# Kernel optimization log

Measured on AMD Instinct MI355X. Metric: run time of the kernel, lower is better.

The kernel has to match this reference:

```python
import jax, jax.numpy as jnp
import numpy as np

V, B, S = 24, 8, 512
H1, H2 = 128, 64          # mechanism hidden sizes
SH1, SH2 = 256, 128       # structure learner hidden sizes
IH = 32                   # independence test hidden
P = V * V                 # all ordered pairs (diag unused)


def _lin(k, fi, fo):
    return jax.random.normal(k, (fi, fo), dtype=jnp.float32) / np.sqrt(fi)


def setup_inputs() -> dict:
    key = jax.random.key(0)
    ks = jax.random.split(key, 18)
    data = jax.random.normal(ks[0], (B, S, V), dtype=jnp.float32)
    # structure learner: V*V -> 256 -> 128 -> V*V
    sW1, sb1 = _lin(ks[1], V * V, SH1), jnp.zeros((SH1,), jnp.float32)
    sW2, sb2 = _lin(ks[2], SH1, SH2), jnp.zeros((SH2,), jnp.float32)
    sW3, sb3 = _lin(ks[3], SH2, V * V), jnp.zeros((V * V,), jnp.float32)
    # per-variable causal mechanisms: (V-1) -> 128 -> 64 -> 1, batched over V
    mW1 = jax.random.normal(ks[4], (V, V - 1, H1), jnp.float32) / np.sqrt(V - 1)
    mb1 = jnp.zeros((V, H1), jnp.float32)
    mW2 = jax.random.normal(ks[5], (V, H1, H2), jnp.float32) / np.sqrt(H1)
    mb2 = jnp.zeros((V, H2), jnp.float32)
    mW3 = jax.random.normal(ks[6], (V, H2, 1), jnp.float32) / np.sqrt(H2)
    mb3 = jnp.zeros((V, 1), jnp.float32)
    # per-pair independence tests: 2 -> 32 -> 1, batched over P pairs
    iW1 = jax.random.normal(ks[7], (P, 2, IH), jnp.float32) / np.sqrt(2)
    ib1 = jnp.zeros((P, IH), jnp.float32)
    iW2 = jax.random.normal(ks[8], (P, IH, 1), jnp.float32) / np.sqrt(IH)
    ib2 = jnp.zeros((P, 1), jnp.float32)
    return dict(data=data, sW1=sW1, sb1=sb1, sW2=sW2, sb2=sb2, sW3=sW3, sb3=sb3,
                mW1=mW1, mb1=mb1, mW2=mW2, mb2=mb2, mW3=mW3, mb3=mb3,
                iW1=iW1, ib1=ib1, iW2=iW2, ib2=ib2)


# constant gather index: others[v] = all variable indices except v (order preserved)
_OTHERS = np.array([[j for j in range(V) if j != v] for v in range(V)])  # [V, V-1]
_II = np.repeat(np.arange(V), V)  # pair -> i
_JJ = np.tile(np.arange(V), V)    # pair -> j


def reference(data, sW1, sb1, sW2, sb2, sW3, sb3,
              mW1, mb1, mW2, mb2, mW3, mb3,
              iW1, ib1, iW2, ib2):
    relu, sig = jax.nn.relu, jax.nn.sigmoid
    b, s, v = data.shape

    # ---- correlations (vectorized torch.corrcoef over all pairs) ----
    avg = data.mean(axis=0)                       # [S, V]
    c = avg - avg.mean(axis=0, keepdims=True)
    cov = c.T @ c                                 # [V, V]
    std = jnp.sqrt(jnp.diag(cov))
    corr = jnp.abs(cov / (std[:, None] * std[None, :]))
    corr = jnp.where(jnp.isnan(corr), 0.0, corr)
    corr = corr * (1.0 - jnp.eye(v, dtype=corr.dtype))

    # ---- structure learner (dropout in eval mode = identity) ----
    h = relu(corr.reshape(1, -1) @ sW1 + sb1)
    h = relu(h @ sW2 + sb2)
    adj = sig(h @ sW3 + sb3).reshape(v, v)
    adj = jnp.triu(adj, k=1)                      # DAG: strict upper triangle

    # ---- causal mechanisms: parent-masked other-vars -> small MLP per var ----
    parent_mask = adj > 0.5                       # parent_mask[p, child]
    x_others = data[:, :, _OTHERS]                # [B, S, V, V-1]
    pmask = parent_mask[_OTHERS, np.arange(V)[:, None]]  # [V, V-1]
    xin = x_others * pmask.astype(data.dtype)[None, None]
    hm = relu(jnp.einsum('bsvf,vfh->bsvh', xin, mW1) + mb1)
    hm = relu(jnp.einsum('bsvh,vhg->bsvg', hm, mW2) + mb2)
    pred = (jnp.einsum('bsvg,vgo->bsvo', hm, mW3) + mb3)[..., 0]  # [B, S, V]
    has_parent = parent_mask.any(axis=0)          # [V]
    predictions = jnp.where(has_parent[None, None, :], pred, data)

    # ---- independence tests: per-pair 2->32->1 MLP, mean over all samples ----
    flatd = data.reshape(b * s, v)                # [N, V]
    tin = jnp.stack([flatd[:, _II], flatd[:, _JJ]], axis=-1)  # [N, P, 2]
    tin = tin.transpose(1, 0, 2)                  # [P, N, 2]
    hi = relu(jnp.einsum('pnf,pfh->pnh', tin, iW1) + ib1[:, None, :])
    si = sig(jnp.einsum('pnh,pho->pno', hi, iW2) + ib2[:, None, :])
    ind_scores = si.mean(axis=(1, 2)).reshape(v, v)

    return adj, predictions, ind_scores
```

## Files before the change

kernel.cpp:

```cpp
#include <hip/hip_runtime.h>
#include <math.h>

#define NV 24
#define NB 8
#define NS 512
#define NTOK 4096
#define H1 128
#define H2 64
#define SH1 256
#define SH2 128
#define IH 32
#define NP 576

typedef short bf16x8 __attribute__((ext_vector_type(8)));
typedef float f32x4 __attribute__((ext_vector_type(4)));

__device__ __forceinline__ short f2bf(float f) {
    union { float f; unsigned u; } x; x.f = f;
    unsigned r = x.u + 0x7fffu + ((x.u >> 16) & 1u);
    return (short)(r >> 16);
}

__device__ __forceinline__ float blk_reduce(float x, float* red, int t) {
#pragma unroll
    for (int o = 32; o > 0; o >>= 1) x += __shfl_xor(x, o);
    if ((t & 63) == 0) red[t >> 6] = x;
    __syncthreads();
    float r = red[0] + red[1] + red[2] + red[3];
    __syncthreads();
    return r;
}


__global__ __launch_bounds__(256) void k_prep(
    const float* __restrict__ data, float* __restrict__ dataT,
    const float* __restrict__ sW1, const float* __restrict__ sW2,
    const float* __restrict__ sW3,
    float* __restrict__ sW1T, float* __restrict__ sW2T, float* __restrict__ sW3T,
    const float* __restrict__ mW1, const float* __restrict__ mW2,
    const float* __restrict__ iW1, const float* __restrict__ ib1,
    const float* __restrict__ iW2,
    float* __restrict__ scratch) {
    __shared__ __align__(16) char L[16900];
    const int u = blockIdx.x, t = threadIdx.x;
    if (u < 384) {
        int idx = u * 256 + t;
        int n = idx / NV, v = idx % NV;
        dataT[v * NTOK + n] = data[idx];
        return;
    }
    if (u < 446) {
        float (*T)[65] = (float (*)[65])L;
        int rb = u - 384;
        const float* src; float* dst; int R, C, ti, tj;
        if (rb < 36)      { src = sW1; dst = sW1T; R = 576; C = 256; ti = rb >> 2;        tj = rb & 3; }
        else if (rb < 44) { src = sW2; dst = sW2T; R = 256; C = 128; ti = (rb - 36) >> 1; tj = (rb - 36) & 1; }
        else              { src = sW3; dst = sW3T; R = 128; C = 576; ti = (rb - 44) / 9;  tj = (rb - 44) % 9; }
        const int col = t & 63, rq = t >> 6;
#pragma unroll
        for (int i = 0; i < 16; ++i) {
            int row = i * 4 + rq;
            T[row][col] = src[(ti * 64 + row) * C + tj * 64 + col];
        }
        __syncthreads();
#pragma unroll
        for (int i = 0; i < 16; ++i) {
            int row = i * 4 + rq;
            dst[(tj * 64 + row) * R + ti * 64 + col] = T[col][row];
        }
        return;
    }
    const int wb = u - 446;
    float acc = 0.f;
    const float4* srcs[5] = { (const float4*)mW1, (const float4*)mW2,
                              (const float4*)iW1, (const float4*)ib1,
                              (const float4*)iW2 };
    const int len4[5] = { NV * 23 * H1 / 4, NV * H1 * H2 / 4,
                          NP * 2 * IH / 4, NP * IH / 4, NP * IH / 4 };
#pragma unroll
    for (int a = 0; a < 5; ++a) {
        const float4* p = srcs[a];
        const int n4 = len4[a];
        for (int idx = wb * 256 + t; idx < n4; idx += 128 * 256) {
            float4 v = p[idx];
            acc += v.x + v.y + v.z + v.w;
        }
    }
    float* red = (float*)L;
    acc = blk_reduce(acc, red, t);
    if (t == 0) scratch[wb] = acc;
}

__global__ __launch_bounds__(256) void k_cov(const float* __restrict__ dataT,
                                             float* __restrict__ cov) {
    __shared__ float red[256];
    const int bx = blockIdx.x;
    const int t = threadIdx.x;
    int i = bx / NV, j = bx % NV;
    const float* ri = dataT + i * NTOK;
    const float* rj = dataT + j * NTOK;
    float ai0 = 0.f, ai1 = 0.f, aj0 = 0.f, aj1 = 0.f;
#pragma unroll
    for (int b = 0; b < NB; ++b) {
        ai0 += ri[b * NS + t];       ai1 += ri[b * NS + t + 256];
        aj0 += rj[b * NS + t];       aj1 += rj[b * NS + t + 256];
    }
    ai0 *= 0.125f; ai1 *= 0.125f; aj0 *= 0.125f; aj1 *= 0.125f;
    float si = blk_reduce(ai0 + ai1, red, t);
    float sj = blk_reduce(aj0 + aj1, red, t);
    float mi = si * (1.f / NS), mj = sj * (1.f / NS);
    float sd = (ai0 - mi) * (aj0 - mj) + (ai1 - mi) * (aj1 - mj);
    sd = blk_reduce(sd, red, t);
    if (t == 0) cov[bx] = sd;
}

__global__ __launch_bounds__(256) void k_adj1(
    const float* __restrict__ cov, const float* __restrict__ sW1T,
    const float* __restrict__ sb1, float* __restrict__ h1out) {
    __shared__ float corrL[NP];
    __shared__ float stdL[NV];
    __shared__ float red[256];
    const int o = blockIdx.x, t = threadIdx.x;
    if (t < NV) stdL[t] = sqrtf(cov[t * (NV + 1)]);
    __syncthreads();
    for (int k = t; k < NP; k += 256) {
        int i = k / NV, j = k % NV;
        float q = fabsf(cov[k] / (stdL[i] * stdL[j]));
        if (isnan(q)) q = 0.f;
        if (i == j) q = 0.f;
        corrL[k] = q;
    }
    __syncthreads();
    const float* w = sW1T + o * 576;
    float w0 = w[t], w1 = w[256 + t];
    float w2 = (t < 64) ? w[512 + t] : 0.f;
    float c2 = (t < 64) ? corrL[512 + t] : 0.f;
    float a = corrL[t] * w0 + corrL[256 + t] * w1 + c2 * w2;
    a = blk_reduce(a, red, t);
    if (t == 0) h1out[o] = fmaxf(a + sb1[o], 0.f);
}

__global__ __launch_bounds__(256) void k_adj2(
    const float* __restrict__ h1, const float* __restrict__ sW2T,
    const float* __restrict__ sb2, float* __restrict__ h2out) {
    __shared__ float red[256];
    const int o = blockIdx.x, t = threadIdx.x;
    float a = h1[t] * sW2T[o * 256 + t];
    a = blk_reduce(a, red, t);
    if (t == 0) h2out[o] = fmaxf(a + sb2[o], 0.f);
}

__global__ __launch_bounds__(256) void k_adj3(
    const float* __restrict__ h2, const float* __restrict__ sW3T,
    const float* __restrict__ sb3, float* __restrict__ out_adj) {
    __shared__ float red[256];
    const int oo = blockIdx.x, t = threadIdx.x;
    float a = (t < SH2) ? h2[t] * sW3T[oo * 128 + t] : 0.f;
    a = blk_reduce(a, red, t);
    if (t == 0) {
        float sg = 1.f / (1.f + expf(-(a + sb3[oo])));
        int i = oo / NV, j = oo % NV;
        out_adj[oo] = (j > i) ? sg : 0.f;
    }
}

__global__ __launch_bounds__(256) void k_predind(
    const float* __restrict__ data,
    const float* __restrict__ mW1, const float* __restrict__ mb1,
    const float* __restrict__ mW2, const float* __restrict__ mb2,
    const float* __restrict__ mW3, const float* __restrict__ mb3,
    const float* __restrict__ adj, float* __restrict__ out_pred,
    const float* __restrict__ dataT,
    const float* __restrict__ iW1, const float* __restrict__ ib1,
    const float* __restrict__ iW2, const float* __restrict__ ib2,
    float* __restrict__ out_ind) {
    __shared__ __align__(16) char L[34816];
    const int bx = blockIdx.x;
    const int t = threadIdx.x;

    if (bx < 768) {
        const int v = bx % NV;
        const int chunk = bx / NV;

        bool hp = false;
#pragma unroll
        for (int r = 0; r < NV; ++r) hp = hp || (adj[r * NV + v] > 0.5f);
        if (!hp) {
            if (t < 128) {
                int tok = chunk * 128 + t;
                out_pred[tok * NV + v] = data[tok * NV + v];
            }
            return;
        }
        short* Xl = (short*)L;
        short* WH = (short*)(L + 10240);
        short* W1B = WH;
        short* W2B = WH + 4096;
        short* Hl = WH;

        if (t < 128) {
            int tok = chunk * 128 + t;
            const float4* dr4 = (const float4*)(data + tok * NV);
            float d[24];
#pragma unroll
            for (int q = 0; q < 6; ++q) {
                float4 uu = dr4[q];
                d[q * 4 + 0] = uu.x; d[q * 4 + 1] = uu.y; d[q * 4 + 2] = uu.z; d[q * 4 + 3] = uu.w;
            }
            short xr[32];
#pragma unroll
            for (int j = 0; j < 23; ++j) {
                int src = j + (j >= v ? 1 : 0);
                xr[j] = f2bf(d[src]);
            }
            xr[23] = f2bf(1.0f);
#pragma unroll
            for (int j = 24; j < 32; ++j) xr[j] = 0;
            short* xp = Xl + t * 40;
#pragma unroll
            for (int q = 0; q < 4; ++q)
                *(bf16x8*)(xp + q * 8) = *(bf16x8*)(xr + q * 8);
        }
        if (t < 184) {
            int k = t >> 3, h8 = (t & 7) * 16;
            int src = k + (k >= v ? 1 : 0);
            float pm = (adj[src * NV + v] > 0.5f) ? 1.f : 0.f;
            const float4* wr = (const float4*)(mW1 + (v * 23 + k) * 128 + h8);
            float wv[16];
#pragma unroll
            for (int q = 0; q < 4; ++q) {
                float4 uu = wr[q];
                wv[q * 4 + 0] = uu.x; wv[q * 4 + 1] = uu.y;
                wv[q * 4 + 2] = uu.z; wv[q * 4 + 3] = uu.w;
            }
            int kb = (k >> 3) & 3, e = k & 7;
#pragma unroll
            for (int q = 0; q < 16; ++q) {
                int h = h8 + q;
                int nt = h >> 4, nn = h & 15;
                W1B[((nt * 4 + kb) * 16 + nn) * 8 + e] = f2bf(wv[q] * pm);
            }
        } else if (t < 200) {
            int h8 = (t - 184) * 8;
            const float4* br = (const float4*)(mb1 + v * 128 + h8);
            float bv[8];
#pragma unroll
            for (int q = 0; q < 2; ++q) {
                float4 uu = br[q];
                bv[q * 4 + 0] = uu.x; bv[q * 4 + 1] = uu.y;
                bv[q * 4 + 2] = uu.z; bv[q * 4 + 3] = uu.w;
            }
#pragma unroll
            for (int q = 0; q < 8; ++q) {
                int h = h8 + q;
                int nt = h >> 4, nn = h & 15;
                W1B[((nt * 4 + 2) * 16 + nn) * 8 + 7] = f2bf(bv[q]);
            }
        }
        if (t < 128) {
            int nt = t >> 4, nn = t & 15;
#pragma unroll
            for (int e = 0; e < 8; ++e)
                W1B[((nt * 4 + 3) * 16 + nn) * 8 + e] = 0;
        }
        {
            int k = t >> 1, n0 = (t & 1) * 32;
            const float4* wr = (const float4*)(mW2 + (v * 128 + k) * 64 + n0);
            float wv[32];
#pragma unroll
            for (int q = 0; q < 8; ++q) {
                float4 uu = wr[q];
                wv[q * 4 + 0] = uu.x; wv[q * 4 + 1] = uu.y;
                wv[q * 4 + 2] = uu.z; wv[q * 4 + 3] = uu.w;
            }
            int s = k >> 5, kb = (k >> 3) & 3, e = k & 7;
#pragma unroll
            for (int q = 0; q < 32; ++q) {
                int n = n0 + q;
                int nt = n >> 4, nn = n & 15;
                W2B[(((s * 4 + nt) * 4 + kb) * 16 + nn) * 8 + e] = f2bf(wv[q]);
            }
        }
        __syncthreads();

        const int lane = t & 63;
        const int wid = t >> 6;
        const int ml = lane & 15;
        const int kb = lane >> 4;
        short* Hw = Hl + wid * 2048;

        bf16x8 w1f[8], w2f[16];
#pragma unroll
        for (int nt = 0; nt < 8; ++nt)
            w1f[nt] = *(bf16x8*)(W1B + (nt * 64 + lane) * 8);
#pragma unroll
        for (int q = 0; q < 16; ++q)
            w2f[q] = *(bf16x8*)(W2B + (q * 64 + lane) * 8);

        float b2r[4], w3r[4];
#pragma unroll
        for (int nt = 0; nt < 4; ++nt) {
            b2r[nt] = mb2[v * 64 + nt * 16 + ml];
            w3r[nt] = mW3[v * 64 + nt * 16 + ml];
        }
        float b3v = mb3[v];

        __syncthreads();

#pragma unroll
        for (int mt = 0; mt < 2; ++mt) {
            int lt = wid * 32 + mt * 16 + ml;
            bf16x8 a1 = *(bf16x8*)(Xl + lt * 40 + kb * 8);
            f32x4 c1[8] = {};
#pragma unroll
            for (int nt = 0; nt < 8; ++nt)
                c1[nt] = __builtin_amdgcn_mfma_f32_16x16x32_bf16(a1, w1f[nt], c1[nt], 0, 0, 0);
#pragma unroll
            for (int nt = 0; nt < 8; ++nt) {
#pragma unroll
                for (int r = 0; r < 4; ++r) {
                    int m = kb * 4 + r;
                    int h = nt * 16 + ml;
                    int bo = (m * 256 + h * 2) ^ ((m & 7) << 4);
                    *(short*)((char*)Hw + bo) = f2bf(fmaxf(c1[nt][r], 0.f));
                }
            }
            f32x4 c2[4] = {};
#pragma unroll
            for (int s = 0; s < 4; ++s) {
                int c0 = s * 32 + kb * 8;
                int bo = (ml * 256 + c0 * 2) ^ ((ml & 7) << 4);
                bf16x8 a2 = *(bf16x8*)((char*)Hw + bo);
#pragma unroll
                for (int nt = 0; nt < 4; ++nt)
                    c2[nt] = __builtin_amdgcn_mfma_f32_16x16x32_bf16(a2, w2f[s * 4 + nt], c2[nt], 0, 0, 0);
            }
            float sacc[4] = {0.f, 0.f, 0.f, 0.f};
#pragma unroll
            for (int nt = 0; nt < 4; ++nt) {
#pragma unroll
                for (int r = 0; r < 4; ++r)
                    sacc[r] += fmaxf(c2[nt][r] + b2r[nt], 0.f) * w3r[nt];
            }
#pragma unroll
            for (int o = 1; o < 16; o <<= 1) {
#pragma unroll
                for (int r = 0; r < 4; ++r)
                    sacc[r] += __shfl_xor(sacc[r], o);
            }
            if (ml == 0) {
                int tokb = chunk * 128 + wid * 32 + mt * 16 + kb * 4;
#pragma unroll
                for (int r = 0; r < 4; ++r)
                    out_pred[(tokb + r) * NV + v] = sacc[r] + b3v;
            }
        }
    } else {
        int p = bx - 768;
        int i = p / NV, j = p % NV;
        float* red = (float*)L;
        float* wl = (float*)L + 256;
        if (t < IH) {
            wl[t]      = iW1[p * 2 * IH + t];
            wl[32 + t] = iW1[p * 2 * IH + IH + t];
            wl[64 + t] = ib1[p * IH + t];
            wl[96 + t] = iW2[p * IH + t];
        }
        __syncthreads();
        float b2v = ib2[p];
        const float* di_p = dataT + i * NTOK;
        const float* dj_p = dataT + j * NTOK;
        float di[16], dj[16], s[16];
#pragma unroll
        for (int q = 0; q < 16; ++q) {
            di[q] = di_p[q * 256 + t];
            dj[q] = dj_p[q * 256 + t];
            s[q] = b2v;
        }
#pragma unroll 4
        for (int h = 0; h < IH; ++h) {
            float w0 = wl[h], w1 = wl[32 + h], bb = wl[64 + h], w2 = wl[96 + h];
#pragma unroll
            for (int q = 0; q < 16; ++q) {
                float a = fmaf(di[q], w0, fmaf(dj[q], w1, bb));
                a = fmaxf(a, 0.f);
                s[q] = fmaf(a, w2, s[q]);
            }
        }
        float acc = 0.f;
#pragma unroll
        for (int q = 0; q < 16; ++q) acc += 1.f / (1.f + expf(-s[q]));
        __syncthreads();
        red[t] = acc;
        __syncthreads();
        for (int st = 128; st > 0; st >>= 1) {
            if (t < st) red[t] += red[t + st];
            __syncthreads();
        }
        if (t == 0) out_ind[p] = red[0] * (1.f / NTOK);
    }
}

extern "C" void kernel_launch(void* const* d_in, const int* in_sizes, int n_in,
                              void* d_out, int out_size, void* d_ws, size_t ws_size,
                              hipStream_t stream) {
    const float* data = (const float*)d_in[0];
    const float* sW1 = (const float*)d_in[1];
    const float* sb1 = (const float*)d_in[2];
    const float* sW2 = (const float*)d_in[3];
    const float* sb2 = (const float*)d_in[4];
    const float* sW3 = (const float*)d_in[5];
    const float* sb3 = (const float*)d_in[6];
    const float* mW1 = (const float*)d_in[7];
    const float* mb1 = (const float*)d_in[8];
    const float* mW2 = (const float*)d_in[9];
    const float* mb2 = (const float*)d_in[10];
    const float* mW3 = (const float*)d_in[11];
    const float* mb3 = (const float*)d_in[12];
    const float* iW1 = (const float*)d_in[13];
    const float* ib1 = (const float*)d_in[14];
    const float* iW2 = (const float*)d_in[15];
    const float* ib2 = (const float*)d_in[16];

    float* out = (float*)d_out;
    float* ws = (float*)d_ws;
    float* ws_cov = ws;
    float* ws_h1 = ws + 576;
    float* ws_h2 = ws + 832;
    float* ws_scratch = ws + 960;
    float* ws_dataT = ws + 2048;
    float* ws_sW1T = ws + 100352;
    float* ws_sW2T = ws + 247808;
    float* ws_sW3T = ws + 280576;

    k_prep<<<dim3(574), dim3(256), 0, stream>>>(data, ws_dataT, sW1, sW2, sW3,
                                                ws_sW1T, ws_sW2T, ws_sW3T,
                                                mW1, mW2, iW1, ib1, iW2,
                                                ws_scratch);
    k_cov<<<dim3(NP), dim3(256), 0, stream>>>(ws_dataT, ws_cov);
    k_adj1<<<dim3(SH1), dim3(256), 0, stream>>>(ws_cov, ws_sW1T, sb1, ws_h1);
    k_adj2<<<dim3(SH2), dim3(256), 0, stream>>>(ws_h1, ws_sW2T, sb2, ws_h2);
    k_adj3<<<dim3(NP), dim3(256), 0, stream>>>(ws_h2, ws_sW3T, sb3, out);
    k_predind<<<dim3(768 + NP), dim3(256), 0, stream>>>(
        data, mW1, mb1, mW2, mb2, mW3, mb3, out, out + NP,
        ws_dataT, iW1, ib1, iW2, ib2, out + NP + NTOK * NV);
}
```

Measured before the change: 43.99 us.

## Fold covariance into prep via partial Gram sums and fuse adj3 into predind

```diff
diff --git a/kernel.cpp b/kernel.cpp
--- a/kernel.cpp
+++ b/kernel.cpp
@@ -40,7 +40,8 @@
     const float* __restrict__ mW1, const float* __restrict__ mW2,
     const float* __restrict__ iW1, const float* __restrict__ ib1,
     const float* __restrict__ iW2,
-    float* __restrict__ scratch) {
+    float* __restrict__ scratch,
+    float* __restrict__ partialS, float* __restrict__ partialG) {
     __shared__ __align__(16) char L[16900];
     const int u = blockIdx.x, t = threadIdx.x;
     if (u < 384) {
@@ -70,62 +71,82 @@
         }
         return;
     }
-    const int wb = u - 446;
-    float acc = 0.f;
-    const float4* srcs[5] = { (const float4*)mW1, (const float4*)mW2,
-                              (const float4*)iW1, (const float4*)ib1,
-                              (const float4*)iW2 };
-    const int len4[5] = { NV * 23 * H1 / 4, NV * H1 * H2 / 4,
-                          NP * 2 * IH / 4, NP * IH / 4, NP * IH / 4 };
-#pragma unroll
-    for (int a = 0; a < 5; ++a) {
-        const float4* p = srcs[a];
-        const int n4 = len4[a];
-        for (int idx = wb * 256 + t; idx < n4; idx += 128 * 256) {
-            float4 v = p[idx];
-            acc += v.x + v.y + v.z + v.w;
-        }
-    }
-    float* red = (float*)L;
-    acc = blk_reduce(acc, red, t);
-    if (t == 0) scratch[wb] = acc;
-}
-
-__global__ __launch_bounds__(256) void k_cov(const float* __restrict__ dataT,
-                                             float* __restrict__ cov) {
-    __shared__ float red[256];
-    const int bx = blockIdx.x;
-    const int t = threadIdx.x;
-    int i = bx / NV, j = bx % NV;
-    const float* ri = dataT + i * NTOK;
-    const float* rj = dataT + j * NTOK;
-    float ai0 = 0.f, ai1 = 0.f, aj0 = 0.f, aj1 = 0.f;
-#pragma unroll
-    for (int b = 0; b < NB; ++b) {
-        ai0 += ri[b * NS + t];       ai1 += ri[b * NS + t + 256];
-        aj0 += rj[b * NS + t];       aj1 += rj[b * NS + t + 256];
-    }
-    ai0 *= 0.125f; ai1 *= 0.125f; aj0 *= 0.125f; aj1 *= 0.125f;
-    float si = blk_reduce(ai0 + ai1, red, t);
-    float sj = blk_reduce(aj0 + aj1, red, t);
-    float mi = si * (1.f / NS), mj = sj * (1.f / NS);
-    float sd = (ai0 - mi) * (aj0 - mj) + (ai1 - mi) * (aj1 - mj);
-    sd = blk_reduce(sd, red, t);
-    if (t == 0) cov[bx] = sd;
+    if (u < 574) {
+        const int wb = u - 446;
+        float acc = 0.f;
+        const float4* srcs[5] = { (const float4*)mW1, (const float4*)mW2,
+                                  (const float4*)iW1, (const float4*)ib1,
+                                  (const float4*)iW2 };
+        const int len4[5] = { NV * 23 * H1 / 4, NV * H1 * H2 / 4,
+                              NP * 2 * IH / 4, NP * IH / 4, NP * IH / 4 };
+#pragma unroll
+        for (int a = 0; a < 5; ++a) {
+            const float4* p = srcs[a];
+            const int n4 = len4[a];
+            for (int idx = wb * 256 + t; idx < n4; idx += 128 * 256) {
+                float4 v = p[idx];
+                acc += v.x + v.y + v.z + v.w;
+            }
+        }
+        float* red = (float*)L;
+        acc = blk_reduce(acc, red, t);
+        if (t == 0) scratch[wb] = acc;
+        return;
+    }
+    const int gb = u - 574;
+    float* avgL = (float*)L;
+    const int s0 = gb * 64;
+    for (int idx = t; idx < 64 * NV; idx += 256) {
+        float a = 0.f;
+#pragma unroll
+        for (int b = 0; b < NB; ++b)
+            a += data[(b * NS + s0) * NV + idx];
+        avgL[idx] = a * 0.125f;
+    }
+    __syncthreads();
+    if (t < NV) {
+        float s = 0.f;
+        for (int ss = 0; ss < 64; ++ss) s += avgL[ss * NV + t];
+        partialS[gb * NV + t] = s;
+    }
+    for (int p = t; p < NP; p += 256) {
+        int i = p / NV, j = p % NV;
+        float g = 0.f;
+        for (int ss = 0; ss < 64; ++ss)
+            g = fmaf(avgL[ss * NV + i], avgL[ss * NV + j], g);
+        partialG[gb * NP + p] = g;
+    }
 }
 
 __global__ __launch_bounds__(256) void k_adj1(
-    const float* __restrict__ cov, const float* __restrict__ sW1T,
-    const float* __restrict__ sb1, float* __restrict__ h1out) {
+    const float* __restrict__ partialG, const float* __restrict__ partialS,
+    const float* __restrict__ sW1T, const float* __restrict__ sb1,
+    float* __restrict__ h1out) {
     __shared__ float corrL[NP];
     __shared__ float stdL[NV];
+    __shared__ float Sv[NV];
     __shared__ float red[256];
     const int o = blockIdx.x, t = threadIdx.x;
-    if (t < NV) stdL[t] = sqrtf(cov[t * (NV + 1)]);
+    if (t < NV) {
+        float s = 0.f;
+#pragma unroll
+        for (int b = 0; b < NB; ++b) s += partialS[b * NV + t];
+        Sv[t] = s;
+    }
+    __syncthreads();
+    for (int k = t; k < NP; k += 256) {
+        float g = 0.f;
+#pragma unroll
+        for (int b = 0; b < NB; ++b) g += partialG[b * NP + k];
+        int i = k / NV, j = k % NV;
+        corrL[k] = g - Sv[i] * Sv[j] * (1.f / NS);
+    }
+    __syncthreads();
+    if (t < NV) stdL[t] = sqrtf(corrL[t * (NV + 1)]);
     __syncthreads();
     for (int k = t; k < NP; k += 256) {
         int i = k / NV, j = k % NV;
-        float q = fabsf(cov[k] / (stdL[i] * stdL[j]));
+        float q = fabsf(corrL[k] / (stdL[i] * stdL[j]));
         if (isnan(q)) q = 0.f;
         if (i == j) q = 0.f;
         corrL[k] = q;
@@ -150,26 +171,14 @@
     if (t == 0) h2out[o] = fmaxf(a + sb2[o], 0.f);
 }
 
-__global__ __launch_bounds__(256) void k_adj3(
-    const float* __restrict__ h2, const float* __restrict__ sW3T,
-    const float* __restrict__ sb3, float* __restrict__ out_adj) {
-    __shared__ float red[256];
-    const int oo = blockIdx.x, t = threadIdx.x;
-    float a = (t < SH2) ? h2[t] * sW3T[oo * 128 + t] : 0.f;
-    a = blk_reduce(a, red, t);
-    if (t == 0) {
-        float sg = 1.f / (1.f + expf(-(a + sb3[oo])));
-        int i = oo / NV, j = oo % NV;
-        out_adj[oo] = (j > i) ? sg : 0.f;
-    }
-}
-
 __global__ __launch_bounds__(256) void k_predind(
     const float* __restrict__ data,
     const float* __restrict__ mW1, const float* __restrict__ mb1,
     const float* __restrict__ mW2, const float* __restrict__ mb2,
     const float* __restrict__ mW3, const float* __restrict__ mb3,
-    const float* __restrict__ adj, float* __restrict__ out_pred,
+    const float* __restrict__ h2, const float* __restrict__ sW3T,
+    const float* __restrict__ sb3,
+    float* __restrict__ out_adj, float* __restrict__ out_pred,
     const float* __restrict__ dataT,
     const float* __restrict__ iW1, const float* __restrict__ ib1,
     const float* __restrict__ iW2, const float* __restrict__ ib2,
@@ -182,9 +191,43 @@
         const int v = bx % NV;
         const int chunk = bx / NV;
 
+        float* P3 = (float*)L;
+        float* maskL = (float*)L + 192;
+        {
+            const int r3 = t >> 3, kq3 = t & 7;
+            if (r3 < NV) {
+                float a = 0.f;
+                if (r3 < v) {
+                    const float* w = sW3T + (r3 * NV + v) * 128 + kq3 * 16;
+                    const float* hp2 = h2 + kq3 * 16;
+#pragma unroll
+                    for (int kk = 0; kk < 16; ++kk)
+                        a = fmaf(hp2[kk], w[kk], a);
+                }
+                P3[r3 * 8 + kq3] = a;
+            }
+        }
+        __syncthreads();
+        if (t < NV) {
+            float s = 0.f;
+#pragma unroll
+            for (int q = 0; q < 8; ++q) s += P3[t * 8 + q];
+            float sg = 1.f / (1.f + expf(-(s + sb3[t * NV + v])));
+            maskL[t] = (t < v && sg > 0.5f) ? 1.f : 0.f;
+        }
+        __syncthreads();
         bool hp = false;
 #pragma unroll
-        for (int r = 0; r < NV; ++r) hp = hp || (adj[r * NV + v] > 0.5f);
+        for (int r = 0; r < NV; ++r) hp = hp || (maskL[r] > 0.5f);
+        float pm_reg = 0.f;
+        int src1 = 0;
+        if (t < 184) {
+            int k = t >> 3;
+            src1 = k + (k >= v ? 1 : 0);
+            pm_reg = maskL[src1];
+        }
+        __syncthreads();
+
         if (!hp) {
             if (t < 128) {
                 int tok = chunk * 128 + t;
@@ -223,8 +266,6 @@
         }
         if (t < 184) {
             int k = t >> 3, h8 = (t & 7) * 16;
-            int src = k + (k >= v ? 1 : 0);
-            float pm = (adj[src * NV + v] > 0.5f) ? 1.f : 0.f;
             const float4* wr = (const float4*)(mW1 + (v * 23 + k) * 128 + h8);
             float wv[16];
 #pragma unroll
@@ -238,7 +279,7 @@
             for (int q = 0; q < 16; ++q) {
                 int h = h8 + q;
                 int nt = h >> 4, nn = h & 15;
-                W1B[((nt * 4 + kb) * 16 + nn) * 8 + e] = f2bf(wv[q] * pm);
+                W1B[((nt * 4 + kb) * 16 + nn) * 8 + e] = f2bf(wv[q] * pm_reg);
             }
         } else if (t < 200) {
             int h8 = (t - 184) * 8;
@@ -355,7 +396,7 @@
                     out_pred[(tokb + r) * NV + v] = sacc[r] + b3v;
             }
         }
-    } else {
+    } else if (bx < 1344) {
         int p = bx - 768;
         int i = p / NV, j = p % NV;
         float* red = (float*)L;
@@ -398,6 +439,16 @@
             __syncthreads();
         }
         if (t == 0) out_ind[p] = red[0] * (1.f / NTOK);
+    } else {
+        float* red = (float*)L;
+        const int oo = bx - 1344;
+        float a = (t < SH2) ? h2[t] * sW3T[oo * 128 + t] : 0.f;
+        a = blk_reduce(a, red, t);
+        if (t == 0) {
+            float sg = 1.f / (1.f + expf(-(a + sb3[oo])));
+            int i = oo / NV, j = oo % NV;
+            out_adj[oo] = (j > i) ? sg : 0.f;
+        }
     }
 }
 
@@ -424,24 +475,23 @@
 
     float* out = (float*)d_out;
     float* ws = (float*)d_ws;
-    float* ws_cov = ws;
     float* ws_h1 = ws + 576;
     float* ws_h2 = ws + 832;
     float* ws_scratch = ws + 960;
-    float* ws_dataT = ws + 2048;
-    float* ws_sW1T = ws + 100352;
-    float* ws_sW2T = ws + 247808;
-    float* ws_sW3T = ws + 280576;
-
-    k_prep<<<dim3(574), dim3(256), 0, stream>>>(data, ws_dataT, sW1, sW2, sW3,
+    float* ws_pS = ws + 1088;
+    float* ws_pG = ws + 1280;
+    float* ws_dataT = ws + 8192;
+    float* ws_sW1T = ws + 106496;
+    float* ws_sW2T = ws + 253952;
+    float* ws_sW3T = ws + 286720;
+
+    k_prep<<<dim3(582), dim3(256), 0, stream>>>(data, ws_dataT, sW1, sW2, sW3,
                                                 ws_sW1T, ws_sW2T, ws_sW3T,
                                                 mW1, mW2, iW1, ib1, iW2,
-                                                ws_scratch);
-    k_cov<<<dim3(NP), dim3(256), 0, stream>>>(ws_dataT, ws_cov);
-    k_adj1<<<dim3(SH1), dim3(256), 0, stream>>>(ws_cov, ws_sW1T, sb1, ws_h1);
+                                                ws_scratch, ws_pS, ws_pG);
+    k_adj1<<<dim3(SH1), dim3(256), 0, stream>>>(ws_pG, ws_pS, ws_sW1T, sb1, ws_h1);
     k_adj2<<<dim3(SH2), dim3(256), 0, stream>>>(ws_h1, ws_sW2T, sb2, ws_h2);
-    k_adj3<<<dim3(NP), dim3(256), 0, stream>>>(ws_h2, ws_sW3T, sb3, out);
-    k_predind<<<dim3(768 + NP), dim3(256), 0, stream>>>(
-        data, mW1, mb1, mW2, mb2, mW3, mb3, out, out + NP,
-        ws_dataT, iW1, ib1, iW2, ib2, out + NP + NTOK * NV);
-}
+    k_predind<<<dim3(768 + NP + NP), dim3(256), 0, stream>>>(
+        data, mW1, mb1, mW2, mb2, mW3, mb3, ws_h2, ws_sW3T, sb3,
+        out, out + NP, ws_dataT, iW1, ib1, iW2, ib2, out + NP + NTOK * NV);
+}
```

New measurement: 42.40 us. 1.04x faster.
